# Performance work log

Hardware: AMD Instinct MI355X
Metric: run time of the kernel (lower is better)

The kernel has to match this reference:

```python
import jax, jax.numpy as jnp
import numpy as np
import math

BLKQ = 64
BLKK = 32
TOPK_FRAC = 0.1


def setup_inputs() -> dict:
    key = jax.random.key(0)
    k1, k2, k3, k4, k5 = jax.random.split(key, 5)
    B, L, H, D = 1, 8192, 16, 64
    q = jax.random.normal(k1, (B, L, H, D), jnp.float32)
    k = jax.random.normal(k2, (B, L, H, D), jnp.float32)
    v = jax.random.normal(k3, (B, L, H, D), jnp.float32)
    # proj_l initialized with nn.init.normal_ (std=1) in the original
    W_proj = jax.random.normal(k4, (D, D), jnp.float32)
    b_proj = jax.random.normal(k5, (D,), jnp.float32)
    return {"q": q, "k": k, "v": v, "W_proj": W_proj, "b_proj": b_proj}


def reference(q, k, v, W_proj, b_proj):
    B, L, H, D = q.shape
    lcm = BLKQ * BLKK // math.gcd(BLKQ, BLKK)
    L_pad = ((L + lcm - 1) // lcm) * lcm
    pad = L_pad - L
    scale = 1.0 / math.sqrt(D)

    # [B, L, H, D] -> [B, H, L_pad, D], zero padded (fused_transpose_pad)
    qt = jnp.transpose(q, (0, 2, 1, 3))
    kt = jnp.transpose(k, (0, 2, 1, 3))
    vt = jnp.transpose(v, (0, 2, 1, 3))
    if pad:
        pw = ((0, 0), (0, 0), (0, pad), (0, 0))
        qt_p = jnp.pad(qt, pw); kt_p = jnp.pad(kt, pw); vt_p = jnp.pad(vt, pw)
    else:
        qt_p, kt_p, vt_p = qt, kt, vt

    # key smoothing (SAGE): subtract per-(b,h) mean of padded k
    km = kt_p.mean(axis=-2, keepdims=True)          # [B, H, 1, D]
    kc = kt_p - km

    M = L_pad // BLKQ
    N = L_pad // BLKK
    # block pooling for routing scores
    pooled_q = qt_p.reshape(B, H, M, BLKQ, D).mean(axis=3)   # [B,H,M,D]
    pooled_k = kc.reshape(B, H, N, BLKK, D).mean(axis=3)     # [B,H,N,D]
    score = jnp.einsum('bhmd,bhnd->bhmn', pooled_q, pooled_k)

    T = min(N, int(TOPK_FRAC * N))                  # real_topk (static)
    _, idx = jax.lax.top_k(score, T)                # [B,H,M,T]
    lut = jnp.sort(idx, axis=-1)

    # gather selected key/value blocks: [B,H,M,T,BLKK,D]
    kb = kc.reshape(B, H, N, BLKK, D)
    vb = vt_p.reshape(B, H, N, BLKK, D)
    kg = jnp.take_along_axis(kb[:, :, None], lut[..., None, None], axis=3)
    vg = jnp.take_along_axis(vb[:, :, None], lut[..., None, None], axis=3)

    qb = qt_p.reshape(B, H, M, BLKQ, D)
    # block-sparse scores: [B,H,M,BLKQ,T,BLKK]
    s = jnp.einsum('bhmqd,bhmtkd->bhmqtk', qb, kg) * scale
    key_pos = lut[..., None] * BLKK + jnp.arange(BLKK)       # [B,H,M,T,BLKK]
    valid = key_pos < L
    s = jnp.where(valid[:, :, :, None, :, :], s, -jnp.inf)
    s = s.reshape(B, H, M, BLKQ, T * BLKK)
    p = jax.nn.softmax(s, axis=-1)
    o_s = jnp.einsum('bhmqn,bhmnd->bhmqd', p, vg.reshape(B, H, M, T * BLKK, D))
    o_s = o_s.reshape(B, H, L_pad, D)[:, :, :L]              # slice to seq_len

    # linear attention branch (softmax feature map over D)
    q_fm = jax.nn.softmax(qt_p[:, :, :L], axis=-1)
    k_fm = jax.nn.softmax(kt_p[:, :, :L], axis=-1)
    kvsum = jnp.einsum('bhld,bhle->bhde', k_fm, vt)          # [B,H,D,D]
    ksum = k_fm.sum(axis=-2)                                 # [B,H,D]
    denom = jnp.einsum('bhld,bhd->bhl', q_fm, ksum)[..., None] + 1e-6
    o_l = jnp.einsum('bhld,bhde->bhle', q_fm, kvsum) / denom
    o_l = o_l @ W_proj.T + b_proj                            # proj_l

    o = jnp.transpose(o_l + o_s, (0, 2, 1, 3))               # [B,L,H,D]
    return o
```

## Files before the change

### kernel.cpp

```cpp
#include <hip/hip_runtime.h>
#include <math.h>

#define SEQL 8192
#define NH 16
#define HD 1024
#define TSEL 25

#define OFF_KVPART 0
#define OFF_KSUM   262144
#define OFF_ZEND   263168
#define OFF_PK     263168
#define OFF_KWT    525312
#define OFF_KSWZ   558080
#define OFF_PQ     0
#define OFF_LUT    131072

typedef __attribute__((ext_vector_type(8))) short bf16x8;
typedef __attribute__((ext_vector_type(4))) float f32x4;

static __device__ inline short f2bf(float f) {
    union { float f; unsigned u; } c; c.f = f;
    unsigned r = (c.u + 0x7FFFu + ((c.u >> 16) & 1u)) >> 16;
    return (short)r;
}
static __device__ inline bf16x8 cvt8(float4 a, float4 b) {
    bf16x8 r;
    r[0] = f2bf(a.x); r[1] = f2bf(a.y); r[2] = f2bf(a.z); r[3] = f2bf(a.w);
    r[4] = f2bf(b.x); r[5] = f2bf(b.y); r[6] = f2bf(b.z); r[7] = f2bf(b.w);
    return r;
}
static __device__ inline void load_lds16(const void* g, void* l) {
    __builtin_amdgcn_global_load_lds((const __attribute__((address_space(1))) unsigned int*)g,
                                     (__attribute__((address_space(3))) unsigned int*)l,
                                     16, 0, 0);
}

__global__ __launch_bounds__(256) void prep_kv(const float* __restrict__ k,
                                               const float* __restrict__ v,
                                               short* __restrict__ kswz,
                                               short* __restrict__ vswz,
                                               float* __restrict__ pk) {
    __shared__ float pcol[4][64];
    int b = blockIdx.x;
    int h = b >> 8, n = b & 255;
    int t = threadIdx.x;
    {
        int r = t >> 3, ch = t & 7;
        const float* src = k + (size_t)(n * 32 + r) * HD + h * 64 + ch * 8;
        float4 f0 = *(const float4*)src, f1 = *(const float4*)(src + 4);
        int f = r * 8 + (ch ^ (r & 7));
        *(bf16x8*)(kswz + (size_t)b * 2048 + f * 8) = cvt8(f0, f1);
        float s[8] = { f0.x, f0.y, f0.z, f0.w, f1.x, f1.y, f1.z, f1.w };
        #pragma unroll
        for (int j = 0; j < 8; j++) {
            s[j] += __shfl_xor(s[j], 8, 64);
            s[j] += __shfl_xor(s[j], 16, 64);
            s[j] += __shfl_xor(s[j], 32, 64);
        }
        if ((t & 63) < 8) {
            #pragma unroll
            for (int j = 0; j < 8; j++) pcol[t >> 6][(t & 7) * 8 + j] = s[j];
        }
    }
    {
        int c = t >> 6, d = t & 63;
        const float* src = v + (size_t)(n * 32 + c * 8) * HD + h * 64 + d;
        bf16x8 val;
        #pragma unroll
        for (int j = 0; j < 8; j++) val[j] = f2bf(src[(size_t)j * HD]);
        int f = d * 4 + (c ^ ((d >> 1) & 3));
        *(bf16x8*)(vswz + (size_t)b * 2048 + f * 8) = val;
    }
    __syncthreads();
    if (t < 64)
        pk[(size_t)b * 64 + t] =
            (pcol[0][t] + pcol[1][t] + pcol[2][t] + pcol[3][t]) * (1.f / 32.f);
}

__global__ void pool_q(const float* __restrict__ q, float* __restrict__ pq) {
    int b = blockIdx.x;
    int h = b >> 7, m = b & 127, d = threadIdx.x;
    const float* base = q + (size_t)m * 64 * HD + h * 64 + d;
    float s = 0.f;
    #pragma unroll 8
    for (int r = 0; r < 64; r++) s += base[(size_t)r * HD];
    pq[(size_t)b * 64 + d] = s * (1.f / 64.f);
}

__global__ __launch_bounds__(256) void score_topk(const float* __restrict__ pq,
                                                  const float* __restrict__ pk,
                                                  int* __restrict__ lut) {
    __shared__ float pq_s[64];
    __shared__ float s_s[256];
    __shared__ int flag[256];
    int b = blockIdx.x;
    int h = b >> 7;
    int t = threadIdx.x;
    if (t < 64) pq_s[t] = pq[(size_t)b * 64 + t];
    __syncthreads();
    const float* kr = pk + ((size_t)h * 256 + t) * 64;
    double acc = 0.0;
    #pragma unroll 8
    for (int d = 0; d < 64; d++) acc += (double)pq_s[d] * (double)kr[d];
    float sc = (float)acc;
    s_s[t] = sc;
    __syncthreads();
    int cnt = 0;
    float si = s_s[t];
    for (int j = 0; j < 256; j++) {
        float sj = s_s[j];
        cnt += (sj > si) || (sj == si && j < t);
    }
    flag[t] = (cnt < TSEL) ? 1 : 0;
    __syncthreads();
    if (cnt < TSEL) {
        int pos = 0;
        for (int j = 0; j < t; j++) pos += flag[j];
        lut[(size_t)b * TSEL + pos] = t;
    }
}

__global__ __launch_bounds__(256) void lin_kv(const float* __restrict__ k,
                                              const float* __restrict__ v,
                                              float* __restrict__ kvpart,
                                              float* __restrict__ ksum) {
    __shared__ float kf[64][68];
    __shared__ float vv[64][68];
    int b = blockIdx.x;
    int h = b >> 7, chunk = b & 127;
    int l0 = chunk * 64;
    int t = threadIdx.x;
    int row = t >> 2, d0 = (t & 3) * 16;
    const float4* ks4 = (const float4*)(k + (size_t)(l0 + row) * HD + h * 64 + d0);
    const float4* vs4 = (const float4*)(v + (size_t)(l0 + row) * HD + h * 64 + d0);
    {
        float4* vd = (float4*)&vv[row][d0];
        #pragma unroll
        for (int i = 0; i < 4; i++) vd[i] = vs4[i];
    }
    float4 X0 = ks4[0], X1 = ks4[1], X2 = ks4[2], X3 = ks4[3];
    float mx = fmaxf(fmaxf(fmaxf(X0.x, X0.y), fmaxf(X0.z, X0.w)),
                     fmaxf(fmaxf(X1.x, X1.y), fmaxf(X1.z, X1.w)));
    mx = fmaxf(mx, fmaxf(fmaxf(fmaxf(X2.x, X2.y), fmaxf(X2.z, X2.w)),
                         fmaxf(fmaxf(X3.x, X3.y), fmaxf(X3.z, X3.w))));
    mx = fmaxf(mx, __shfl_xor(mx, 1, 64));
    mx = fmaxf(mx, __shfl_xor(mx, 2, 64));
    X0.x = __expf(X0.x - mx); X0.y = __expf(X0.y - mx); X0.z = __expf(X0.z - mx); X0.w = __expf(X0.w - mx);
    X1.x = __expf(X1.x - mx); X1.y = __expf(X1.y - mx); X1.z = __expf(X1.z - mx); X1.w = __expf(X1.w - mx);
    X2.x = __expf(X2.x - mx); X2.y = __expf(X2.y - mx); X2.z = __expf(X2.z - mx); X2.w = __expf(X2.w - mx);
    X3.x = __expf(X3.x - mx); X3.y = __expf(X3.y - mx); X3.z = __expf(X3.z - mx); X3.w = __expf(X3.w - mx);
    float sm = (X0.x + X0.y + X0.z + X0.w) + (X1.x + X1.y + X1.z + X1.w)
             + (X2.x + X2.y + X2.z + X2.w) + (X3.x + X3.y + X3.z + X3.w);
    sm += __shfl_xor(sm, 1, 64);
    sm += __shfl_xor(sm, 2, 64);
    float inv = 1.f / sm;
    X0.x *= inv; X0.y *= inv; X0.z *= inv; X0.w *= inv;
    X1.x *= inv; X1.y *= inv; X1.z *= inv; X1.w *= inv;
    X2.x *= inv; X2.y *= inv; X2.z *= inv; X2.w *= inv;
    X3.x *= inv; X3.y *= inv; X3.z *= inv; X3.w *= inv;
    {
        float4* kd = (float4*)&kf[row][d0];
        kd[0] = X0; kd[1] = X1; kd[2] = X2; kd[3] = X3;
    }
    __syncthreads();
    int e_ = t & 63, dg = t >> 6;
    float acc[16];
    #pragma unroll
    for (int j = 0; j < 16; j++) acc[j] = 0.f;
    for (int l = 0; l < 64; l++) {
        float vl = vv[l][e_];
        const float4* k4 = (const float4*)&kf[l][dg * 16];
        float4 a = k4[0], b4 = k4[1], c4 = k4[2], d4 = k4[3];
        acc[0]  += a.x * vl;  acc[1]  += a.y * vl;  acc[2]  += a.z * vl;  acc[3]  += a.w * vl;
        acc[4]  += b4.x * vl; acc[5]  += b4.y * vl; acc[6]  += b4.z * vl; acc[7]  += b4.w * vl;
        acc[8]  += c4.x * vl; acc[9]  += c4.y * vl; acc[10] += c4.z * vl; acc[11] += c4.w * vl;
        acc[12] += d4.x * vl; acc[13] += d4.y * vl; acc[14] += d4.z * vl; acc[15] += d4.w * vl;
    }
    float* dst = kvpart + ((size_t)(chunk & 3) * 16 + h) * 4096;
    #pragma unroll
    for (int j = 0; j < 16; j++)
        atomicAdd(&dst[(dg * 16 + j) * 64 + e_], acc[j]);
    if (t < 64) {
        float s = 0.f;
        for (int l = 0; l < 64; l++) s += kf[l][t];
        atomicAdd(&ksum[h * 64 + t], s);
    }
}

__global__ __launch_bounds__(256) void kw_mul(const float* __restrict__ kvpart,
                                              const float* __restrict__ W,
                                              short* __restrict__ kwt) {
    __shared__ float kv[64][65];
    __shared__ float w[64][65];
    int h = blockIdx.x, t = threadIdx.x;
    for (int i = t; i < 4096; i += 256) {
        float s = 0.f;
        #pragma unroll
        for (int p = 0; p < 4; p++) s += kvpart[((size_t)p * 16 + h) * 4096 + i];
        kv[i >> 6][i & 63] = s;
        w[i >> 6][i & 63] = W[i];
    }
    __syncthreads();
    int dd = t & 63, dg = t >> 6;
    #pragma unroll
    for (int j = 0; j < 16; j++) {
        int d = dg * 16 + j;
        float a = 0.f;
        #pragma unroll 8
        for (int e = 0; e < 64; e++) a += kv[d][e] * w[dd][e];
        kwt[(size_t)h * 4096 + dd * 64 + d] = f2bf(a);
    }
}

__global__ __launch_bounds__(256) void sparse_attn_mfma(const float* __restrict__ q,
                                                        const short* __restrict__ kswz,
                                                        const short* __restrict__ vswz,
                                                        const int* __restrict__ lut,
                                                        const short* __restrict__ kwt,
                                                        const float* __restrict__ ksum,
                                                        const float* __restrict__ bproj,
                                                        float* __restrict__ out) {
    __shared__ __align__(16) short Kb[2][2048];
    __shared__ __align__(16) short Vb[2][2048];
    __shared__ __align__(16) short Pl[64][40];
    __shared__ int lut_s[TSEL];

    int b = blockIdx.x;
    int x = b & 7, jj = b >> 3;
    int h = x * 2 + (jj >> 7);
    int m = jj & 127;
    int t = threadIdx.x;
    int lane = t & 63, w = t >> 6;
    int l15 = lane & 15, quad = lane >> 4;

    if (t < TSEL) lut_s[t] = lut[(size_t)(h * 128 + m) * TSEL + t];
    __syncthreads();

    {
        size_t base = (size_t)(h * 256 + lut_s[0]) * 2048;
        load_lds16(kswz + base + t * 8, &Kb[0][t * 8]);
        load_lds16(vswz + base + t * 8, &Vb[0][t * 8]);
        load_lds16(kwt + (size_t)h * 4096 + t * 8, &Kb[1][t * 8]);
        load_lds16(kwt + (size_t)h * 4096 + 2048 + t * 8, &Vb[1][t * 8]);
    }

    const float* qrow = q + (size_t)(m * 64 + w * 16 + l15) * HD + h * 64;
    float4 x0 = *(const float4*)(qrow + quad * 8);
    float4 x1 = *(const float4*)(qrow + quad * 8 + 4);
    float4 x2 = *(const float4*)(qrow + 32 + quad * 8);
    float4 x3 = *(const float4*)(qrow + 32 + quad * 8 + 4);
    bf16x8 qa[2];
    qa[0] = cvt8(x0, x1);
    qa[1] = cvt8(x2, x3);

    float mx = fmaxf(fmaxf(fmaxf(x0.x, x0.y), fmaxf(x0.z, x0.w)),
                     fmaxf(fmaxf(x1.x, x1.y), fmaxf(x1.z, x1.w)));
    mx = fmaxf(mx, fmaxf(fmaxf(fmaxf(x2.x, x2.y), fmaxf(x2.z, x2.w)),
                         fmaxf(fmaxf(x3.x, x3.y), fmaxf(x3.z, x3.w))));
    mx = fmaxf(mx, __shfl_xor(mx, 16, 64));
    mx = fmaxf(mx, __shfl_xor(mx, 32, 64));
    x0.x = __expf(x0.x - mx); x0.y = __expf(x0.y - mx); x0.z = __expf(x0.z - mx); x0.w = __expf(x0.w - mx);
    x1.x = __expf(x1.x - mx); x1.y = __expf(x1.y - mx); x1.z = __expf(x1.z - mx); x1.w = __expf(x1.w - mx);
    x2.x = __expf(x2.x - mx); x2.y = __expf(x2.y - mx); x2.z = __expf(x2.z - mx); x2.w = __expf(x2.w - mx);
    x3.x = __expf(x3.x - mx); x3.y = __expf(x3.y - mx); x3.z = __expf(x3.z - mx); x3.w = __expf(x3.w - mx);
    float sm = (x0.x + x0.y + x0.z + x0.w) + (x1.x + x1.y + x1.z + x1.w)
             + (x2.x + x2.y + x2.z + x2.w) + (x3.x + x3.y + x3.z + x3.w);
    sm += __shfl_xor(sm, 16, 64);
    sm += __shfl_xor(sm, 32, 64);
    float qsc = 1.f / sm;
    float4 ka0 = *(const float4*)(ksum + h * 64 + quad * 8);
    float4 ka1 = *(const float4*)(ksum + h * 64 + quad * 8 + 4);
    float4 ka2 = *(const float4*)(ksum + h * 64 + 32 + quad * 8);
    float4 ka3 = *(const float4*)(ksum + h * 64 + 32 + quad * 8 + 4);
    float dq = x0.x * ka0.x + x0.y * ka0.y + x0.z * ka0.z + x0.w * ka0.w
             + x1.x * ka1.x + x1.y * ka1.y + x1.z * ka1.z + x1.w * ka1.w
             + x2.x * ka2.x + x2.y * ka2.y + x2.z * ka2.z + x2.w * ka2.w
             + x3.x * ka3.x + x3.y * ka3.y + x3.z * ka3.z + x3.w * ka3.w;
    dq += __shfl_xor(dq, 16, 64);
    dq += __shfl_xor(dq, 32, 64);
    float invd = 1.f / (dq * qsc + 1e-6f);
    x0.x *= qsc; x0.y *= qsc; x0.z *= qsc; x0.w *= qsc;
    x1.x *= qsc; x1.y *= qsc; x1.z *= qsc; x1.w *= qsc;
    x2.x *= qsc; x2.y *= qsc; x2.z *= qsc; x2.w *= qsc;
    x3.x *= qsc; x3.y *= qsc; x3.z *= qsc; x3.w *= qsc;
    bf16x8 qf[2];
    qf[0] = cvt8(x0, x1);
    qf[1] = cvt8(x2, x3);

    __syncthreads();

    f32x4 Ol[4];
    #pragma unroll
    for (int dt = 0; dt < 4; dt++) Ol[dt] = (f32x4){0.f, 0.f, 0.f, 0.f};
    #pragma unroll
    for (int dt = 0; dt < 4; dt++) {
        #pragma unroll
        for (int kc = 0; kc < 2; kc++) {
            int flat = (dt * 16 + l15) * 64 + kc * 32 + quad * 8;
            bf16x8 a = (dt < 2) ? *(const bf16x8*)&Kb[1][flat]
                                : *(const bf16x8*)&Vb[1][flat - 2048];
            Ol[dt] = __builtin_amdgcn_mfma_f32_16x16x32_bf16(a, qf[kc], Ol[dt], 0, 0, 0);
        }
    }

    f32x4 O[4];
    #pragma unroll
    for (int dt = 0; dt < 4; dt++) O[dt] = (f32x4){0.f, 0.f, 0.f, 0.f};
    float l_i = 0.f;
    const f32x4 z = (f32x4){0.f, 0.f, 0.f, 0.f};

    for (int ti = 0; ti < TSEL; ti++) {
        __syncthreads();
        int buf = ti & 1;
        if (ti + 1 < TSEL) {
            size_t base = (size_t)(h * 256 + lut_s[ti + 1]) * 2048;
            load_lds16(kswz + base + t * 8, &Kb[buf ^ 1][t * 8]);
            load_lds16(vswz + base + t * 8, &Vb[buf ^ 1][t * 8]);
        }
        int r0 = l15, r1 = 16 + l15;
        bf16x8 a00 = *(const bf16x8*)&Kb[buf][(r0 * 8 + (quad ^ (r0 & 7))) * 8];
        bf16x8 a01 = *(const bf16x8*)&Kb[buf][(r0 * 8 + ((4 + quad) ^ (r0 & 7))) * 8];
        bf16x8 a10 = *(const bf16x8*)&Kb[buf][(r1 * 8 + (quad ^ (r1 & 7))) * 8];
        bf16x8 a11 = *(const bf16x8*)&Kb[buf][(r1 * 8 + ((4 + quad) ^ (r1 & 7))) * 8];
        f32x4 s0 = __builtin_amdgcn_mfma_f32_16x16x32_bf16(a00, qa[0], z, 0, 0, 0);
        s0 = __builtin_amdgcn_mfma_f32_16x16x32_bf16(a01, qa[1], s0, 0, 0, 0);
        f32x4 s1 = __builtin_amdgcn_mfma_f32_16x16x32_bf16(a10, qa[0], z, 0, 0, 0);
        s1 = __builtin_amdgcn_mfma_f32_16x16x32_bf16(a11, qa[1], s1, 0, 0, 0);

        float p0[4], p1[4];
        float lsum = 0.f;
        #pragma unroll
        for (int r = 0; r < 4; r++) {
            p0[r] = __expf(s0[r] * 0.125f);
            p1[r] = __expf(s1[r] * 0.125f);
            lsum += p0[r] + p1[r];
        }
        lsum += __shfl_xor(lsum, 16, 64);
        lsum += __shfl_xor(lsum, 32, 64);
        l_i += lsum;

        #pragma unroll
        for (int r = 0; r < 4; r++) {
            Pl[w * 16 + l15][quad * 4 + r] = f2bf(p0[r]);
            Pl[w * 16 + l15][16 + quad * 4 + r] = f2bf(p1[r]);
        }

        asm volatile("s_waitcnt lgkmcnt(0)\n\ts_barrier" ::: "memory");

        bf16x8 pb = *(const bf16x8*)&Pl[w * 16 + l15][quad * 8];
        #pragma unroll
        for (int dt = 0; dt < 4; dt++) {
            int d = dt * 16 + l15;
            bf16x8 va = *(const bf16x8*)&Vb[buf][(d * 4 + (quad ^ ((d >> 1) & 3))) * 8];
            O[dt] = __builtin_amdgcn_mfma_f32_16x16x32_bf16(va, pb, O[dt], 0, 0, 0);
        }
    }

    float inv = 1.f / l_i;
    float* dst = out + (size_t)(m * 64 + w * 16 + l15) * HD + h * 64;
    #pragma unroll
    for (int dt = 0; dt < 4; dt++) {
        float4 bv = *(const float4*)(bproj + dt * 16 + quad * 4);
        float4 o;
        o.x = O[dt][0] * inv + Ol[dt][0] * invd + bv.x;
        o.y = O[dt][1] * inv + Ol[dt][1] * invd + bv.y;
        o.z = O[dt][2] * inv + Ol[dt][2] * invd + bv.z;
        o.w = O[dt][3] * inv + Ol[dt][3] * invd + bv.w;
        *(float4*)(dst + dt * 16 + quad * 4) = o;
    }
}

extern "C" void kernel_launch(void* const* d_in, const int* in_sizes, int n_in,
                              void* d_out, int out_size, void* d_ws, size_t ws_size,
                              hipStream_t stream) {
    const float* q  = (const float*)d_in[0];
    const float* k  = (const float*)d_in[1];
    const float* v  = (const float*)d_in[2];
    const float* W  = (const float*)d_in[3];
    const float* bp = (const float*)d_in[4];
    float* out = (float*)d_out;
    float* ws = (float*)d_ws;

    float* kvpart = ws + OFF_KVPART;
    float* ksum   = ws + OFF_KSUM;
    float* pk     = ws + OFF_PK;
    short* kwt    = (short*)(ws + OFF_KWT);
    short* kswz   = (short*)(ws + OFF_KSWZ);
    short* vswz   = kswz + (size_t)16 * 256 * 2048;
    float* pq     = ws + OFF_PQ;
    int*   lut    = (int*)(ws + OFF_LUT);

    hipMemsetAsync(ws, 0, OFF_ZEND * sizeof(float), stream);
    prep_kv<<<4096, 256, 0, stream>>>(k, v, kswz, vswz, pk);
    lin_kv<<<2048, 256, 0, stream>>>(k, v, kvpart, ksum);
    kw_mul<<<16, 256, 0, stream>>>(kvpart, W, kwt);
    pool_q<<<2048, 64, 0, stream>>>(q, pq);
    score_topk<<<2048, 256, 0, stream>>>(pq, pk, lut);
    sparse_attn_mfma<<<2048, 256, 0, stream>>>(q, kswz, vswz, lut, kwt, ksum, bp, out);
}
```

Before: 289.9 us.

## Retile lin_kv and kw_mul, ballot-based topk compaction, faster exp/pack in attention

Several independent changes land together. lin_kv now has each block process four 32-row chunks with a 4x4 register tile over (d,e), halving the grid and the atomic traffic. kw_mul is split across four blocks per head with float4 dot products. score_topk replaces the serial prefix scan with wave ballot and popcount, and reads scores as float4. The sparse attention loop uses exp2 with a pre-folded scale, packed bf16 conversion, and s_setprio around MFMA groups. Risks are small rounding differences from the new exp and conversion paths, and fewer blocks for lin_kv.

```diff
diff --git a/kernel.cpp b/kernel.cpp
--- a/kernel.cpp
+++ b/kernel.cpp
@@ -28,6 +28,18 @@
     r[0] = f2bf(a.x); r[1] = f2bf(a.y); r[2] = f2bf(a.z); r[3] = f2bf(a.w);
     r[4] = f2bf(b.x); r[5] = f2bf(b.y); r[6] = f2bf(b.z); r[7] = f2bf(b.w);
     return r;
+}
+static __device__ inline unsigned cvtpk(float a, float b) {
+    unsigned r;
+    asm("v_cvt_pk_bf16_f32 %0, %1, %2" : "=v"(r) : "v"(a), "v"(b));
+    return r;
+}
+static __device__ inline float exp2a(float x) {
+#if __has_builtin(__builtin_amdgcn_exp2f)
+    return __builtin_amdgcn_exp2f(x);
+#else
+    float r; asm("v_exp_f32 %0, %1" : "=v"(r) : "v"(x)); return r;
+#endif
 }
 static __device__ inline void load_lds16(const void* g, void* l) {
     __builtin_amdgcn_global_load_lds((const __attribute__((address_space(1))) unsigned int*)g,
@@ -90,12 +102,13 @@
 __global__ __launch_bounds__(256) void score_topk(const float* __restrict__ pq,
                                                   const float* __restrict__ pk,
                                                   int* __restrict__ lut) {
-    __shared__ float pq_s[64];
-    __shared__ float s_s[256];
-    __shared__ int flag[256];
+    __shared__ __align__(16) float pq_s[64];
+    __shared__ __align__(16) float s_s[256];
+    __shared__ int wcnt[4];
     int b = blockIdx.x;
     int h = b >> 7;
     int t = threadIdx.x;
+    int lane = t & 63, w = t >> 6;
     if (t < 64) pq_s[t] = pq[(size_t)b * 64 + t];
     __syncthreads();
     const float* kr = pk + ((size_t)h * 256 + t) * 64;
@@ -106,17 +119,24 @@
     s_s[t] = sc;
     __syncthreads();
     int cnt = 0;
-    float si = s_s[t];
-    for (int j = 0; j < 256; j++) {
-        float sj = s_s[j];
-        cnt += (sj > si) || (sj == si && j < t);
-    }
-    flag[t] = (cnt < TSEL) ? 1 : 0;
-    __syncthreads();
-    if (cnt < TSEL) {
-        int pos = 0;
-        for (int j = 0; j < t; j++) pos += flag[j];
-        lut[(size_t)b * TSEL + pos] = t;
+    float si = sc;
+    #pragma unroll 4
+    for (int j4 = 0; j4 < 64; j4++) {
+        float4 sv = *(const float4*)&s_s[j4 * 4];
+        int j = j4 * 4;
+        cnt += (sv.x > si) || (sv.x == si && (j + 0) < t);
+        cnt += (sv.y > si) || (sv.y == si && (j + 1) < t);
+        cnt += (sv.z > si) || (sv.z == si && (j + 2) < t);
+        cnt += (sv.w > si) || (sv.w == si && (j + 3) < t);
+    }
+    bool sel = cnt < TSEL;
+    unsigned long long bal = __ballot(sel);
+    if (lane == 0) wcnt[w] = __popcll(bal);
+    __syncthreads();
+    if (sel) {
+        int off = __popcll(bal & ((1ull << lane) - 1ull));
+        for (int i = 0; i < w; i++) off += wcnt[i];
+        lut[(size_t)b * TSEL + off] = t;
     }
 }
 
@@ -124,91 +144,104 @@
                                               const float* __restrict__ v,
                                               float* __restrict__ kvpart,
                                               float* __restrict__ ksum) {
-    __shared__ float kf[64][68];
-    __shared__ float vv[64][68];
+    __shared__ __align__(16) float kf[32][66];
+    __shared__ __align__(16) float vv[32][66];
     int b = blockIdx.x;
-    int h = b >> 7, chunk = b & 127;
-    int l0 = chunk * 64;
+    int h = b >> 6, c0 = b & 63;
     int t = threadIdx.x;
-    int row = t >> 2, d0 = (t & 3) * 16;
-    const float4* ks4 = (const float4*)(k + (size_t)(l0 + row) * HD + h * 64 + d0);
-    const float4* vs4 = (const float4*)(v + (size_t)(l0 + row) * HD + h * 64 + d0);
-    {
-        float4* vd = (float4*)&vv[row][d0];
-        #pragma unroll
-        for (int i = 0; i < 4; i++) vd[i] = vs4[i];
-    }
-    float4 X0 = ks4[0], X1 = ks4[1], X2 = ks4[2], X3 = ks4[3];
-    float mx = fmaxf(fmaxf(fmaxf(X0.x, X0.y), fmaxf(X0.z, X0.w)),
-                     fmaxf(fmaxf(X1.x, X1.y), fmaxf(X1.z, X1.w)));
-    mx = fmaxf(mx, fmaxf(fmaxf(fmaxf(X2.x, X2.y), fmaxf(X2.z, X2.w)),
-                         fmaxf(fmaxf(X3.x, X3.y), fmaxf(X3.z, X3.w))));
-    mx = fmaxf(mx, __shfl_xor(mx, 1, 64));
-    mx = fmaxf(mx, __shfl_xor(mx, 2, 64));
-    X0.x = __expf(X0.x - mx); X0.y = __expf(X0.y - mx); X0.z = __expf(X0.z - mx); X0.w = __expf(X0.w - mx);
-    X1.x = __expf(X1.x - mx); X1.y = __expf(X1.y - mx); X1.z = __expf(X1.z - mx); X1.w = __expf(X1.w - mx);
-    X2.x = __expf(X2.x - mx); X2.y = __expf(X2.y - mx); X2.z = __expf(X2.z - mx); X2.w = __expf(X2.w - mx);
-    X3.x = __expf(X3.x - mx); X3.y = __expf(X3.y - mx); X3.z = __expf(X3.z - mx); X3.w = __expf(X3.w - mx);
-    float sm = (X0.x + X0.y + X0.z + X0.w) + (X1.x + X1.y + X1.z + X1.w)
-             + (X2.x + X2.y + X2.z + X2.w) + (X3.x + X3.y + X3.z + X3.w);
-    sm += __shfl_xor(sm, 1, 64);
-    sm += __shfl_xor(sm, 2, 64);
-    float inv = 1.f / sm;
-    X0.x *= inv; X0.y *= inv; X0.z *= inv; X0.w *= inv;
-    X1.x *= inv; X1.y *= inv; X1.z *= inv; X1.w *= inv;
-    X2.x *= inv; X2.y *= inv; X2.z *= inv; X2.w *= inv;
-    X3.x *= inv; X3.y *= inv; X3.z *= inv; X3.w *= inv;
-    {
-        float4* kd = (float4*)&kf[row][d0];
-        kd[0] = X0; kd[1] = X1; kd[2] = X2; kd[3] = X3;
-    }
-    __syncthreads();
-    int e_ = t & 63, dg = t >> 6;
+    int lane = t & 63, w = t >> 6;
+    int prow = t >> 3, c8 = (t & 7) * 8;
+    int d0 = (lane & 15) * 4, e0 = (lane >> 4) * 4 + w * 16;
     float acc[16];
     #pragma unroll
-    for (int j = 0; j < 16; j++) acc[j] = 0.f;
-    for (int l = 0; l < 64; l++) {
-        float vl = vv[l][e_];
-        const float4* k4 = (const float4*)&kf[l][dg * 16];
-        float4 a = k4[0], b4 = k4[1], c4 = k4[2], d4 = k4[3];
-        acc[0]  += a.x * vl;  acc[1]  += a.y * vl;  acc[2]  += a.z * vl;  acc[3]  += a.w * vl;
-        acc[4]  += b4.x * vl; acc[5]  += b4.y * vl; acc[6]  += b4.z * vl; acc[7]  += b4.w * vl;
-        acc[8]  += c4.x * vl; acc[9]  += c4.y * vl; acc[10] += c4.z * vl; acc[11] += c4.w * vl;
-        acc[12] += d4.x * vl; acc[13] += d4.y * vl; acc[14] += d4.z * vl; acc[15] += d4.w * vl;
-    }
-    float* dst = kvpart + ((size_t)(chunk & 3) * 16 + h) * 4096;
-    #pragma unroll
-    for (int j = 0; j < 16; j++)
-        atomicAdd(&dst[(dg * 16 + j) * 64 + e_], acc[j]);
-    if (t < 64) {
-        float s = 0.f;
-        for (int l = 0; l < 64; l++) s += kf[l][t];
-        atomicAdd(&ksum[h * 64 + t], s);
-    }
+    for (int i = 0; i < 16; i++) acc[i] = 0.f;
+    float ks_acc = 0.f;
+    for (int half = 0; half < 4; half++) {
+        int lr = (c0 + (half >> 1) * 64) * 64 + (half & 1) * 32;
+        const float* ksrc = k + (size_t)(lr + prow) * HD + h * 64 + c8;
+        const float* vsrc = v + (size_t)(lr + prow) * HD + h * 64 + c8;
+        float4 X0 = *(const float4*)ksrc;
+        float4 X1 = *(const float4*)(ksrc + 4);
+        float4 V0 = *(const float4*)vsrc;
+        float4 V1 = *(const float4*)(vsrc + 4);
+        *(float4*)&vv[prow][c8] = V0;
+        *(float4*)&vv[prow][c8 + 4] = V1;
+        float mx = fmaxf(fmaxf(fmaxf(X0.x, X0.y), fmaxf(X0.z, X0.w)),
+                         fmaxf(fmaxf(X1.x, X1.y), fmaxf(X1.z, X1.w)));
+        mx = fmaxf(mx, __shfl_xor(mx, 1, 64));
+        mx = fmaxf(mx, __shfl_xor(mx, 2, 64));
+        mx = fmaxf(mx, __shfl_xor(mx, 4, 64));
+        X0.x = __expf(X0.x - mx); X0.y = __expf(X0.y - mx);
+        X0.z = __expf(X0.z - mx); X0.w = __expf(X0.w - mx);
+        X1.x = __expf(X1.x - mx); X1.y = __expf(X1.y - mx);
+        X1.z = __expf(X1.z - mx); X1.w = __expf(X1.w - mx);
+        float sm = (X0.x + X0.y + X0.z + X0.w) + (X1.x + X1.y + X1.z + X1.w);
+        sm += __shfl_xor(sm, 1, 64);
+        sm += __shfl_xor(sm, 2, 64);
+        sm += __shfl_xor(sm, 4, 64);
+        float inv = 1.f / sm;
+        X0.x *= inv; X0.y *= inv; X0.z *= inv; X0.w *= inv;
+        X1.x *= inv; X1.y *= inv; X1.z *= inv; X1.w *= inv;
+        *(float4*)&kf[prow][c8] = X0;
+        *(float4*)&kf[prow][c8 + 4] = X1;
+        __syncthreads();
+        #pragma unroll 8
+        for (int l = 0; l < 32; l++) {
+            float4 kd = *(const float4*)&kf[l][d0];
+            float4 ve = *(const float4*)&vv[l][e0];
+            acc[0]  += kd.x * ve.x; acc[1]  += kd.x * ve.y; acc[2]  += kd.x * ve.z; acc[3]  += kd.x * ve.w;
+            acc[4]  += kd.y * ve.x; acc[5]  += kd.y * ve.y; acc[6]  += kd.y * ve.z; acc[7]  += kd.y * ve.w;
+            acc[8]  += kd.z * ve.x; acc[9]  += kd.z * ve.y; acc[10] += kd.z * ve.z; acc[11] += kd.z * ve.w;
+            acc[12] += kd.w * ve.x; acc[13] += kd.w * ve.y; acc[14] += kd.w * ve.z; acc[15] += kd.w * ve.w;
+        }
+        if (t < 64) {
+            float s = 0.f;
+            #pragma unroll 8
+            for (int l = 0; l < 32; l++) s += kf[l][t];
+            ks_acc += s;
+        }
+        __syncthreads();
+    }
+    float* dst = kvpart + ((size_t)(b & 3) * 16 + h) * 4096;
+    #pragma unroll
+    for (int i = 0; i < 4; i++)
+        #pragma unroll
+        for (int j = 0; j < 4; j++)
+            atomicAdd(&dst[(d0 + i) * 64 + e0 + j], acc[i * 4 + j]);
+    if (t < 64) atomicAdd(&ksum[h * 64 + t], ks_acc);
 }
 
 __global__ __launch_bounds__(256) void kw_mul(const float* __restrict__ kvpart,
                                               const float* __restrict__ W,
                                               short* __restrict__ kwt) {
-    __shared__ float kv[64][65];
-    __shared__ float w[64][65];
-    int h = blockIdx.x, t = threadIdx.x;
-    for (int i = t; i < 4096; i += 256) {
+    __shared__ __align__(16) float kv[16][68];
+    __shared__ __align__(16) float wsm[64][68];
+    int h = blockIdx.x >> 2, dq = blockIdx.x & 3;
+    int t = threadIdx.x;
+    for (int i = t; i < 1024; i += 256) {
+        int dl = i >> 6, e = i & 63;
         float s = 0.f;
         #pragma unroll
-        for (int p = 0; p < 4; p++) s += kvpart[((size_t)p * 16 + h) * 4096 + i];
-        kv[i >> 6][i & 63] = s;
-        w[i >> 6][i & 63] = W[i];
-    }
-    __syncthreads();
-    int dd = t & 63, dg = t >> 6;
-    #pragma unroll
-    for (int j = 0; j < 16; j++) {
-        int d = dg * 16 + j;
+        for (int p = 0; p < 4; p++)
+            s += kvpart[((size_t)p * 16 + h) * 4096 + (dq * 16 + dl) * 64 + e];
+        kv[dl][e] = s;
+    }
+    for (int i = t; i < 4096; i += 256) wsm[i >> 6][i & 63] = W[i];
+    __syncthreads();
+    int lane = t & 63, wi = t >> 6;
+    int dl = lane & 15;
+    int db = wi * 16 + (lane >> 4) * 4;
+    #pragma unroll
+    for (int j = 0; j < 4; j++) {
+        int dd = db + j;
         float a = 0.f;
-        #pragma unroll 8
-        for (int e = 0; e < 64; e++) a += kv[d][e] * w[dd][e];
-        kwt[(size_t)h * 4096 + dd * 64 + d] = f2bf(a);
+        #pragma unroll
+        for (int e4 = 0; e4 < 16; e4++) {
+            float4 kq = *(const float4*)&kv[dl][e4 * 4];
+            float4 wq = *(const float4*)&wsm[dd][e4 * 4];
+            a += kq.x * wq.x + kq.y * wq.y + kq.z * wq.z + kq.w * wq.w;
+        }
+        kwt[(size_t)h * 4096 + dd * 64 + dq * 16 + dl] = f2bf(a);
     }
 }
 
@@ -292,6 +325,7 @@
     f32x4 Ol[4];
     #pragma unroll
     for (int dt = 0; dt < 4; dt++) Ol[dt] = (f32x4){0.f, 0.f, 0.f, 0.f};
+    __builtin_amdgcn_s_setprio(1);
     #pragma unroll
     for (int dt = 0; dt < 4; dt++) {
         #pragma unroll
@@ -302,12 +336,14 @@
             Ol[dt] = __builtin_amdgcn_mfma_f32_16x16x32_bf16(a, qf[kc], Ol[dt], 0, 0, 0);
         }
     }
+    __builtin_amdgcn_s_setprio(0);
 
     f32x4 O[4];
     #pragma unroll
     for (int dt = 0; dt < 4; dt++) O[dt] = (f32x4){0.f, 0.f, 0.f, 0.f};
     float l_i = 0.f;
     const f32x4 z = (f32x4){0.f, 0.f, 0.f, 0.f};
+    const float EC = 1.44269504f * 0.125f;
 
     for (int ti = 0; ti < TSEL; ti++) {
         __syncthreads();
@@ -322,38 +358,42 @@
         bf16x8 a01 = *(const bf16x8*)&Kb[buf][(r0 * 8 + ((4 + quad) ^ (r0 & 7))) * 8];
         bf16x8 a10 = *(const bf16x8*)&Kb[buf][(r1 * 8 + (quad ^ (r1 & 7))) * 8];
         bf16x8 a11 = *(const bf16x8*)&Kb[buf][(r1 * 8 + ((4 + quad) ^ (r1 & 7))) * 8];
+        __builtin_amdgcn_s_setprio(1);
         f32x4 s0 = __builtin_amdgcn_mfma_f32_16x16x32_bf16(a00, qa[0], z, 0, 0, 0);
         s0 = __builtin_amdgcn_mfma_f32_16x16x32_bf16(a01, qa[1], s0, 0, 0, 0);
         f32x4 s1 = __builtin_amdgcn_mfma_f32_16x16x32_bf16(a10, qa[0], z, 0, 0, 0);
         s1 = __builtin_amdgcn_mfma_f32_16x16x32_bf16(a11, qa[1], s1, 0, 0, 0);
+        __builtin_amdgcn_s_setprio(0);
 
         float p0[4], p1[4];
         float lsum = 0.f;
         #pragma unroll
         for (int r = 0; r < 4; r++) {
-            p0[r] = __expf(s0[r] * 0.125f);
-            p1[r] = __expf(s1[r] * 0.125f);
+            p0[r] = exp2a(s0[r] * EC);
+            p1[r] = exp2a(s1[r] * EC);
             lsum += p0[r] + p1[r];
         }
         lsum += __shfl_xor(lsum, 16, 64);
         lsum += __shfl_xor(lsum, 32, 64);
         l_i += lsum;
 
-        #pragma unroll
-        for (int r = 0; r < 4; r++) {
-            Pl[w * 16 + l15][quad * 4 + r] = f2bf(p0[r]);
-            Pl[w * 16 + l15][16 + quad * 4 + r] = f2bf(p1[r]);
-        }
+        uint2 pkA, pkB;
+        pkA.x = cvtpk(p0[0], p0[1]); pkA.y = cvtpk(p0[2], p0[3]);
+        pkB.x = cvtpk(p1[0], p1[1]); pkB.y = cvtpk(p1[2], p1[3]);
+        *(uint2*)&Pl[w * 16 + l15][quad * 4] = pkA;
+        *(uint2*)&Pl[w * 16 + l15][16 + quad * 4] = pkB;
 
         asm volatile("s_waitcnt lgkmcnt(0)\n\ts_barrier" ::: "memory");
 
         bf16x8 pb = *(const bf16x8*)&Pl[w * 16 + l15][quad * 8];
+        __builtin_amdgcn_s_setprio(1);
         #pragma unroll
         for (int dt = 0; dt < 4; dt++) {
             int d = dt * 16 + l15;
             bf16x8 va = *(const bf16x8*)&Vb[buf][(d * 4 + (quad ^ ((d >> 1) & 3))) * 8];
             O[dt] = __builtin_amdgcn_mfma_f32_16x16x32_bf16(va, pb, O[dt], 0, 0, 0);
         }
+        __builtin_amdgcn_s_setprio(0);
     }
 
     float inv = 1.f / l_i;
@@ -392,8 +432,8 @@
 
     hipMemsetAsync(ws, 0, OFF_ZEND * sizeof(float), stream);
     prep_kv<<<4096, 256, 0, stream>>>(k, v, kswz, vswz, pk);
-    lin_kv<<<2048, 256, 0, stream>>>(k, v, kvpart, ksum);
-    kw_mul<<<16, 256, 0, stream>>>(kvpart, W, kwt);
+    lin_kv<<<1024, 256, 0, stream>>>(k, v, kvpart, ksum);
+    kw_mul<<<64, 256, 0, stream>>>(kvpart, W, kwt);
     pool_q<<<2048, 64, 0, stream>>>(q, pq);
     score_topk<<<2048, 256, 0, stream>>>(pq, pk, lut);
     sparse_attn_mfma<<<2048, 256, 0, stream>>>(q, kswz, vswz, lut, kwt, ksum, bp, out);
```

Measured after the change: 314.8 us. 1.09x slower.
